# Kernel tuning notes

Hardware: AMD Instinct MI355X
Metric: run time of the kernel (lower is better)

## Reference

```python
import jax, jax.numpy as jnp
import numpy as np

B, S, V, E, H, L = 16, 256, 32000, 512, 1024, 2


def setup_inputs() -> dict:
    key = jax.random.key(0)
    ks = jax.random.split(key, 10)
    scale = 0.02
    tokens = jax.random.randint(ks[0], (B, S), 1, V)  # avoid pad token 0
    emb = jax.random.normal(ks[1], (V, E), dtype=jnp.float32) * scale
    W0 = jax.random.normal(ks[2], (E, 4 * H), dtype=jnp.float32) * scale
    U0 = jax.random.normal(ks[3], (H, 4 * H), dtype=jnp.float32) * scale
    b0 = jnp.zeros((4 * H,), dtype=jnp.float32)
    W1 = jax.random.normal(ks[4], (H, 4 * H), dtype=jnp.float32) * scale
    U1 = jax.random.normal(ks[5], (H, 4 * H), dtype=jnp.float32) * scale
    b1 = jnp.zeros((4 * H,), dtype=jnp.float32)
    Wd = jax.random.normal(ks[6], (H, V), dtype=jnp.float32) * scale
    bd = jnp.zeros((V,), dtype=jnp.float32)
    return {"tokens": tokens, "emb": emb, "W0": W0, "U0": U0, "b0": b0,
            "W1": W1, "U1": U1, "b1": b1, "Wd": Wd, "bd": bd}


def lstm_layer(x, mask, W, U, b):
    """Keras LSTM (gate order i,f,g,o), mask carries state/output on padded steps.
    x: [B,S,D], mask: [B,S] bool -> (ys [B,S,H], h [B,H], c [B,H])."""
    h_dim = U.shape[0]
    bsz = x.shape[0]
    x_t = jnp.swapaxes(x, 0, 1)           # [S,B,D]
    m_t = jnp.swapaxes(mask, 0, 1)        # [S,B]

    def step(carry, inp):
        h, c = carry
        xt, mt = inp
        z = xt @ W + h @ U + b            # [B,4H]
        i, f, g, o = jnp.split(z, 4, axis=-1)
        c_new = jax.nn.sigmoid(f) * c + jax.nn.sigmoid(i) * jnp.tanh(g)
        h_new = jax.nn.sigmoid(o) * jnp.tanh(c_new)
        mt = mt[:, None]
        h_new = jnp.where(mt, h_new, h)
        c_new = jnp.where(mt, c_new, c)
        return (h_new, c_new), h_new

    init = (jnp.zeros((bsz, h_dim), x.dtype), jnp.zeros((bsz, h_dim), x.dtype))
    (h, c), ys = jax.lax.scan(step, init, (x_t, m_t))
    return jnp.swapaxes(ys, 0, 1), h, c


def reference(tokens, emb, W0, U0, b0, W1, U1, b1, Wd, bd):
    mask = tokens != 0                    # mask_zero=True in Embedding
    x = emb[tokens]                       # [B,S,E]
    x, h0, c0 = lstm_layer(x, mask, W0, U0, b0)
    x, h1, c1 = lstm_layer(x, mask, W1, U1, b1)
    probs = jax.nn.softmax(x @ Wd + bd, axis=-1)  # Dense(softmax) -> [B,S,V]
    h_stack = jnp.stack([h0, h1])         # [L,B,H] final hidden states
    c_stack = jnp.stack([c0, c1])         # [L,B,H] final cell states
    return probs, h_stack, c_stack
```

## Files before the change

### kernel.cpp

```cpp
#include <hip/hip_runtime.h>

typedef __attribute__((ext_vector_type(8))) short bf16x8;
typedef __attribute__((ext_vector_type(4))) float f32x4;

#define S_LEN 256
#define VOCAB 32000
#define EMB   512
#define HID   1024

static const size_t OUT_H = 131072000ull;

__device__ inline unsigned short f2bf(float f) {
  unsigned int u = __float_as_uint(f);
  u = (u + 0x7FFFu + ((u >> 16) & 1u)) >> 16;
  return (unsigned short)u;
}
__device__ inline float bf2f(unsigned short s) {
  return __uint_as_float(((unsigned int)s) << 16);
}

__device__ inline void st_h(unsigned short* p, unsigned short v) {
  __hip_atomic_store(p, v, __ATOMIC_RELAXED, __HIP_MEMORY_SCOPE_AGENT);
}

__device__ inline int xcd_swz(int o, int n) {
  int q = n >> 3, r = n & 7;
  int x = o & 7, i = o >> 3;
  return (x < r ? x * (q + 1) : r * (q + 1) + (x - r) * q) + i;
}

__global__ __launch_bounds__(256) void k_transpose_bf16(const float* __restrict__ src,
                                                        unsigned short* __restrict__ dst,
                                                        int K, int N) {
  __shared__ float tile[64][65];
  int n0 = blockIdx.x * 64, k0 = blockIdx.y * 64;
  int tid = threadIdx.x;
#pragma unroll
  for (int i = 0; i < 16; ++i) {
    int e = tid + i * 256;
    int r = e >> 6, c = e & 63;
    tile[r][c] = src[(size_t)(k0 + r) * N + n0 + c];
  }
  __syncthreads();
#pragma unroll
  for (int i = 0; i < 16; ++i) {
    int e = tid + i * 256;
    int r = e >> 6, c = e & 63;
    dst[(size_t)(n0 + r) * K + k0 + c] = f2bf(tile[c][r]);
  }
}

__global__ __launch_bounds__(256) void k_gather_emb(const int* __restrict__ tokens,
                                                    const float* __restrict__ emb,
                                                    unsigned short* __restrict__ Xg) {
  int r = blockIdx.x;
  int s = r >> 4, b = r & 15;
  int tok = tokens[b * S_LEN + s];
  const float* src = emb + (size_t)tok * EMB;
  int k = threadIdx.x * 2;
  float2 v = *(const float2*)(src + k);
  ushort2 o; o.x = f2bf(v.x); o.y = f2bf(v.y);
  *(ushort2*)(Xg + (size_t)r * EMB + k) = o;
}

__device__ inline void gload16(const void* g, void* lds) {
  __builtin_amdgcn_global_load_lds((const __attribute__((address_space(1))) unsigned int*)g,
                                   (__attribute__((address_space(3))) unsigned int*)lds,
                                   16, 0, 0);
}

template <bool SMPART, bool BF16OUT>
__global__ __launch_bounds__(256) void k_gemm_bf16(const unsigned short* __restrict__ A,
                                                   const unsigned short* __restrict__ BT,
                                                   float* __restrict__ Cf,
                                                   unsigned short* __restrict__ Cb,
                                                   const float* __restrict__ bias,
                                                   int M, int N, int K,
                                                   float* __restrict__ Mpart,
                                                   float* __restrict__ Spart,
                                                   int NT) {
  __shared__ unsigned short As[4096];
  __shared__ unsigned short Bs[4096];
  __shared__ float redM[2][2][64];
  __shared__ float redS[2][2][64];
  int tid = threadIdx.x;
  int lane = tid & 63, wv = tid >> 6;
  int wr = wv >> 1, wc = wv & 1;
  int bxs = xcd_swz(blockIdx.x, gridDim.x);
  int am0 = blockIdx.y * 128, bn0 = bxs * 128;
  f32x4 zero = {0.f, 0.f, 0.f, 0.f};
  f32x4 acc[4][4];
#pragma unroll
  for (int m = 0; m < 4; ++m)
#pragma unroll
    for (int n = 0; n < 4; ++n) acc[m][n] = zero;
  int KT = K >> 5;
  int lr = lane & 15, kq = lane >> 4;
  for (int kt = 0; kt < KT; ++kt) {
    int k0 = kt << 5;
    __syncthreads();
#pragma unroll
    for (int c = 0; c < 2; ++c) {
      int t2 = c * 256 + tid;
      int row = t2 & 127, kg = t2 >> 7;
      gload16(A + (size_t)(am0 + row) * K + k0 + kg * 8, &As[(c * 256 + wv * 64) * 8]);
    }
#pragma unroll
    for (int c = 0; c < 2; ++c) {
      int t2 = c * 256 + tid;
      int row = t2 & 127, kg = t2 >> 7;
      gload16(BT + (size_t)(bn0 + row) * K + k0 + kg * 8, &Bs[(c * 256 + wv * 64) * 8]);
    }
    __syncthreads();
    const bf16x8* Ap = (const bf16x8*)As;
    const bf16x8* Bp = (const bf16x8*)Bs;
    bf16x8 af[4], bf[4];
#pragma unroll
    for (int m = 0; m < 4; ++m) af[m] = Ap[kq * 128 + wr * 64 + m * 16 + lr];
#pragma unroll
    for (int n = 0; n < 4; ++n) bf[n] = Bp[kq * 128 + wc * 64 + n * 16 + lr];
#pragma unroll
    for (int m = 0; m < 4; ++m)
#pragma unroll
      for (int n = 0; n < 4; ++n)
        acc[m][n] = __builtin_amdgcn_mfma_f32_16x16x32_bf16(af[m], bf[n], acc[m][n], 0, 0, 0);
  }
  float bvc[4];
#pragma unroll
  for (int n = 0; n < 4; ++n) {
    int col = bn0 + wc * 64 + n * 16 + lr;
    bvc[n] = bias ? bias[col] : 0.f;
  }
#pragma unroll
  for (int m = 0; m < 4; ++m)
#pragma unroll
    for (int n = 0; n < 4; ++n) {
      int col = bn0 + wc * 64 + n * 16 + lr;
#pragma unroll
      for (int q = 0; q < 4; ++q) {
        int row = am0 + wr * 64 + m * 16 + kq * 4 + q;
        if constexpr (BF16OUT)
          Cb[(size_t)row * N + col] = f2bf(acc[m][n][q] + bvc[n]);
        else
          Cf[(size_t)row * N + col] = acc[m][n][q] + bvc[n];
      }
    }
  if constexpr (SMPART) {
#pragma unroll
    for (int m = 0; m < 4; ++m)
#pragma unroll
      for (int q = 0; q < 4; ++q) {
        float mx = fmaxf(fmaxf(acc[m][0][q] + bvc[0], acc[m][1][q] + bvc[1]),
                         fmaxf(acc[m][2][q] + bvc[2], acc[m][3][q] + bvc[3]));
#pragma unroll
        for (int off = 1; off < 16; off <<= 1) mx = fmaxf(mx, __shfl_xor(mx, off));
        if (lr == 0) redM[wr][wc][m * 16 + kq * 4 + q] = mx;
      }
    __syncthreads();
#pragma unroll
    for (int m = 0; m < 4; ++m)
#pragma unroll
      for (int q = 0; q < 4; ++q) {
        int idx = m * 16 + kq * 4 + q;
        float mxF = fmaxf(redM[wr][0][idx], redM[wr][1][idx]);
        float s = __expf(acc[m][0][q] + bvc[0] - mxF) + __expf(acc[m][1][q] + bvc[1] - mxF) +
                  __expf(acc[m][2][q] + bvc[2] - mxF) + __expf(acc[m][3][q] + bvc[3] - mxF);
#pragma unroll
        for (int off = 1; off < 16; off <<= 1) s += __shfl_xor(s, off);
        if (lr == 0) redS[wr][wc][idx] = s;
      }
    __syncthreads();
    if (wc == 0 && lr == 0) {
#pragma unroll
      for (int m = 0; m < 4; ++m)
#pragma unroll
        for (int q = 0; q < 4; ++q) {
          int idx = m * 16 + kq * 4 + q;
          int row = am0 + wr * 64 + idx;
          Mpart[(size_t)row * NT + bxs] = fmaxf(redM[wr][0][idx], redM[wr][1][idx]);
          Spart[(size_t)row * NT + bxs] = redS[wr][0][idx] + redS[wr][1][idx];
        }
    }
  }
}

__global__ __launch_bounds__(256) void k_sm_combine(const float* __restrict__ Mp,
                                                    const float* __restrict__ Sp,
                                                    float* __restrict__ MS, int T) {
  int row = blockIdx.x * 4 + (threadIdx.x >> 6);
  int lane = threadIdx.x & 63;
  float mx = -3.4e38f;
  for (int i = lane; i < T; i += 64) mx = fmaxf(mx, Mp[(size_t)row * T + i]);
#pragma unroll
  for (int o = 32; o > 0; o >>= 1) mx = fmaxf(mx, __shfl_xor(mx, o));
  float s = 0.f;
  for (int i = lane; i < T; i += 64)
    s += Sp[(size_t)row * T + i] * __expf(Mp[(size_t)row * T + i] - mx);
#pragma unroll
  for (int o = 32; o > 0; o >>= 1) s += __shfl_xor(s, o);
  if (lane == 0) { MS[row * 2] = mx; MS[row * 2 + 1] = 1.f / s; }
}

__global__ __launch_bounds__(256) void k_sm_apply(float* __restrict__ data,
                                                  const float* __restrict__ MS) {
  const int total = 4096 * (VOCAB / 4);
  for (int idx = blockIdx.x * 256 + threadIdx.x; idx < total; idx += gridDim.x * 256) {
    int row = idx / (VOCAB / 4);
    float M = MS[row * 2], inv = MS[row * 2 + 1];
    float4 v = ((const float4*)data)[idx];
    v.x = __expf(v.x - M) * inv;
    v.y = __expf(v.y - M) * inv;
    v.z = __expf(v.z - M) * inv;
    v.w = __expf(v.w - M) * inv;
    ((float4*)data)[idx] = v;
  }
}

__global__ __launch_bounds__(256) void k_sm_apply_bf16(const unsigned short* __restrict__ lg,
                                                       float* __restrict__ probs,
                                                       const float* __restrict__ MS) {
  const int total = 4096 * (VOCAB / 4);
  for (int idx = blockIdx.x * 256 + threadIdx.x; idx < total; idx += gridDim.x * 256) {
    int row = idx / (VOCAB / 4);
    float M = MS[row * 2], inv = MS[row * 2 + 1];
    ushort4 v = ((const ushort4*)lg)[idx];
    float4 o;
    o.x = __expf(bf2f(v.x) - M) * inv;
    o.y = __expf(bf2f(v.y) - M) * inv;
    o.z = __expf(bf2f(v.z) - M) * inv;
    o.w = __expf(bf2f(v.w) - M) * inv;
    ((float4*)probs)[idx] = o;
  }
}

struct LstmSmem {
  unsigned short U0s[16384];
  unsigned short W1s[16384];
  unsigned short U1s[16384];
  float zA[4][16][16];
  float zB[4][16][16];
  float c0[16][4], h0f[16][4], c1[16][4], h1f[16][4];
  float b1s[16];
  short toks[16][256];
  unsigned short h0st[16][4], h1st[16][4];
};

__global__ __launch_bounds__(256, 1) void k_lstm(const int* __restrict__ tokens,
                                                 const float* __restrict__ XW,
                                                 const unsigned short* __restrict__ U0T,
                                                 const unsigned short* __restrict__ W1T,
                                                 const unsigned short* __restrict__ U1T,
                                                 const float* __restrict__ b1,
                                                 unsigned short* __restrict__ h0r,
                                                 unsigned short* __restrict__ h1r,
                                                 unsigned short* __restrict__ Y1,
                                                 float* outHC,
                                                 int* bar) {
  extern __shared__ char smraw[];
  LstmSmem& sm = *(LstmSmem*)smraw;
  int tid = threadIdx.x, bid = blockIdx.x;
  int lane = tid & 63, wv = tid >> 6;

  for (int idx = tid; idx < 2048; idx += 256) {
    int cidx = idx >> 7, kg = idx & 127;
    int gcol = (cidx >> 2) * 1024 + bid * 4 + (cidx & 3);
    *(uint4*)&sm.U0s[(kg * 16 + cidx) * 8] = *(const uint4*)&U0T[(size_t)gcol * 1024 + kg * 8];
    *(uint4*)&sm.W1s[(kg * 16 + cidx) * 8] = *(const uint4*)&W1T[(size_t)gcol * 1024 + kg * 8];
    *(uint4*)&sm.U1s[(kg * 16 + cidx) * 8] = *(const uint4*)&U1T[(size_t)gcol * 1024 + kg * 8];
  }
  for (int idx = tid; idx < 4096; idx += 256) {
    sm.toks[idx >> 8][idx & 255] = (short)tokens[idx];
  }
  if (tid < 64) {
    int b = tid >> 2, u = tid & 3;
    sm.c0[b][u] = 0.f; sm.h0f[b][u] = 0.f;
    sm.c1[b][u] = 0.f; sm.h1f[b][u] = 0.f;
  }
  if (tid < 16) sm.b1s[tid] = b1[(tid >> 2) * 1024 + bid * 4 + (tid & 3)];
  __syncthreads();

  int lr = lane & 15, kq = lane >> 4;

  auto gbar = [&](int gen) {
    __syncthreads();
    if (tid == 0)
      __hip_atomic_store(&bar[bid * 16], gen, __ATOMIC_RELAXED, __HIP_MEMORY_SCOPE_AGENT);
    int ok;
    do {
      int f = __hip_atomic_load(&bar[tid * 16], __ATOMIC_RELAXED, __HIP_MEMORY_SCOPE_AGENT);
      ok = (f >= gen);
    } while (!__syncthreads_and(ok));
  };

  if (wv == 1) {
    int l = tid - 64, b = l >> 2, u = l & 3;
    const float* xp = XW + (size_t)b * 4096 + bid * 4 + u;
    float z0 = xp[0], z2 = xp[2048], z3 = xp[3072];
    float ii = 1.f / (1.f + expf(-z0));
    float gg = tanhf(z2);
    float oo = 1.f / (1.f + expf(-z3));
    float cn = ii * gg;
    float hn = oo * tanhf(cn);
    if (sm.toks[b][0] == 0) { cn = 0.f; hn = 0.f; }
    sm.c0[b][u] = cn; sm.h0f[b][u] = hn;
    st_h(h0r + b * HID + bid * 4 + u, f2bf(hn));
  }
  gbar(1);

  for (int t = 0; t < 255; ++t) {
    const unsigned short* h0t = h0r + (size_t)t * 16384;
    const unsigned short* h1p = h1r + (size_t)(t > 0 ? t - 1 : 0) * 16384;
    unsigned short* h1c = h1r + (size_t)t * 16384;
    unsigned short* h0n = h0r + (size_t)(t + 1) * 16384;

    float xwv0 = 0, xwv1 = 0, xwv2 = 0, xwv3 = 0;
    if (wv == 1) {
      int l = tid - 64, b = l >> 2, u = l & 3;
      const float* xp = XW + ((size_t)(t + 1) * 16 + b) * 4096 + bid * 4 + u;
      xwv0 = xp[0]; xwv1 = xp[1024]; xwv2 = xp[2048]; xwv3 = xp[3072];
    }

    f32x4 accB = {0.f, 0.f, 0.f, 0.f};
    {
      const unsigned short* ap = (wv < 2) ? h0t : h1p;
      const unsigned short* bm = (wv < 2) ? sm.W1s : sm.U1s;
      int kofs = (wv & 1) * 512;
      if (wv < 2 || t > 0) {
#pragma unroll
        for (int s8 = 0; s8 < 16; ++s8) {
          int kb = kofs + s8 * 32;
          bf16x8 av = *(const bf16x8*)(ap + lr * HID + kb + kq * 8);
          bf16x8 bv = *(const bf16x8*)&bm[(((kb >> 3) + kq) * 16 + lr) * 8];
          accB = __builtin_amdgcn_mfma_f32_16x16x32_bf16(av, bv, accB, 0, 0, 0);
        }
      }
    }
    f32x4 accA = {0.f, 0.f, 0.f, 0.f};
#pragma unroll
    for (int s8 = 0; s8 < 8; ++s8) {
      int kb = wv * 256 + s8 * 32;
      bf16x8 av = *(const bf16x8*)(h0t + lr * HID + kb + kq * 8);
      bf16x8 bv = *(const bf16x8*)&sm.U0s[(((kb >> 3) + kq) * 16 + lr) * 8];
      accA = __builtin_amdgcn_mfma_f32_16x16x32_bf16(av, bv, accA, 0, 0, 0);
    }
#pragma unroll
    for (int q = 0; q < 4; ++q) {
      sm.zB[wv][kq * 4 + q][lr] = accB[q];
      sm.zA[wv][kq * 4 + q][lr] = accA[q];
    }
    __syncthreads();

    if (wv == 0) {
      int b = tid >> 2, u = tid & 3;
      int tok = sm.toks[b][t];
      float z0 = sm.b1s[0 + u]  + sm.zB[0][b][0 + u]  + sm.zB[1][b][0 + u]  + sm.zB[2][b][0 + u]  + sm.zB[3][b][0 + u];
      float z1 = sm.b1s[4 + u]  + sm.zB[0][b][4 + u]  + sm.zB[1][b][4 + u]  + sm.zB[2][b][4 + u]  + sm.zB[3][b][4 + u];
      float z2 = sm.b1s[8 + u]  + sm.zB[0][b][8 + u]  + sm.zB[1][b][8 + u]  + sm.zB[2][b][8 + u]  + sm.zB[3][b][8 + u];
      float z3 = sm.b1s[12 + u] + sm.zB[0][b][12 + u] + sm.zB[1][b][12 + u] + sm.zB[2][b][12 + u] + sm.zB[3][b][12 + u];
      float ii = 1.f / (1.f + expf(-z0));
      float ff = 1.f / (1.f + expf(-z1));
      float gg = tanhf(z2);
      float oo = 1.f / (1.f + expf(-z3));
      float cold = sm.c1[b][u], hold = sm.h1f[b][u];
      float cn = ff * cold + ii * gg;
      float hn = oo * tanhf(cn);
      if (tok == 0) { cn = cold; hn = hold; }
      sm.c1[b][u] = cn; sm.h1f[b][u] = hn;
      unsigned short hb = f2bf(hn);
      sm.h1st[b][u] = hb;
      Y1[((size_t)b * S_LEN + t) * HID + bid * 4 + u] = hb;
    } else if (wv == 1) {
      int l = tid - 64, b = l >> 2, u = l & 3;
      int tok = sm.toks[b][t + 1];
      float z0 = xwv0 + sm.zA[0][b][0 + u]  + sm.zA[1][b][0 + u]  + sm.zA[2][b][0 + u]  + sm.zA[3][b][0 + u];
      float z1 = xwv1 + sm.zA[0][b][4 + u]  + sm.zA[1][b][4 + u]  + sm.zA[2][b][4 + u]  + sm.zA[3][b][4 + u];
      float z2 = xwv2 + sm.zA[0][b][8 + u]  + sm.zA[1][b][8 + u]  + sm.zA[2][b][8 + u]  + sm.zA[3][b][8 + u];
      float z3 = xwv3 + sm.zA[0][b][12 + u] + sm.zA[1][b][12 + u] + sm.zA[2][b][12 + u] + sm.zA[3][b][12 + u];
      float ii = 1.f / (1.f + expf(-z0));
      float ff = 1.f / (1.f + expf(-z1));
      float gg = tanhf(z2);
      float oo = 1.f / (1.f + expf(-z3));
      float cold = sm.c0[b][u], hold = sm.h0f[b][u];
      float cn = ff * cold + ii * gg;
      float hn = oo * tanhf(cn);
      if (tok == 0) { cn = cold; hn = hold; }
      sm.c0[b][u] = cn; sm.h0f[b][u] = hn;
      sm.h0st[b][u] = f2bf(hn);
    }
    __syncthreads();
    if (tid < 32) {
      int b = tid & 15;
      unsigned long long v = *(const unsigned long long*)((tid < 16) ? &sm.h1st[b][0]
                                                                     : &sm.h0st[b][0]);
      unsigned short* dst = (tid < 16) ? (h1c + b * HID + bid * 4)
                                       : (h0n + b * HID + bid * 4);
      __hip_atomic_store((unsigned long long*)dst, v, __ATOMIC_RELAXED,
                         __HIP_MEMORY_SCOPE_AGENT);
    }
    gbar(t + 2);
  }

  {
    const unsigned short* h0t = h0r + 255ull * 16384;
    const unsigned short* h1p = h1r + 254ull * 16384;
    f32x4 accB = {0.f, 0.f, 0.f, 0.f};
    const unsigned short* ap = (wv < 2) ? h0t : h1p;
    const unsigned short* bm = (wv < 2) ? sm.W1s : sm.U1s;
    int kofs = (wv & 1) * 512;
#pragma unroll
    for (int s8 = 0; s8 < 16; ++s8) {
      int kb = kofs + s8 * 32;
      bf16x8 av = *(const bf16x8*)(ap + lr * HID + kb + kq * 8);
      bf16x8 bv = *(const bf16x8*)&bm[(((kb >> 3) + kq) * 16 + lr) * 8];
      accB = __builtin_amdgcn_mfma_f32_16x16x32_bf16(av, bv, accB, 0, 0, 0);
    }
#pragma unroll
    for (int q = 0; q < 4; ++q) sm.zB[wv][kq * 4 + q][lr] = accB[q];
    __syncthreads();
    if (wv == 0) {
      int b = tid >> 2, u = tid & 3;
      int tok = sm.toks[b][255];
      float z0 = sm.b1s[0 + u]  + sm.zB[0][b][0 + u]  + sm.zB[1][b][0 + u]  + sm.zB[2][b][0 + u]  + sm.zB[3][b][0 + u];
      float z1 = sm.b1s[4 + u]  + sm.zB[0][b][4 + u]  + sm.zB[1][b][4 + u]  + sm.zB[2][b][4 + u]  + sm.zB[3][b][4 + u];
      float z2 = sm.b1s[8 + u]  + sm.zB[0][b][8 + u]  + sm.zB[1][b][8 + u]  + sm.zB[2][b][8 + u]  + sm.zB[3][b][8 + u];
      float z3 = sm.b1s[12 + u] + sm.zB[0][b][12 + u] + sm.zB[1][b][12 + u] + sm.zB[2][b][12 + u] + sm.zB[3][b][12 + u];
      float ii = 1.f / (1.f + expf(-z0));
      float ff = 1.f / (1.f + expf(-z1));
      float gg = tanhf(z2);
      float oo = 1.f / (1.f + expf(-z3));
      float cold = sm.c1[b][u], hold = sm.h1f[b][u];
      float cn = ff * cold + ii * gg;
      float hn = oo * tanhf(cn);
      if (tok == 0) { cn = cold; hn = hold; }
      sm.c1[b][u] = cn; sm.h1f[b][u] = hn;
      Y1[((size_t)b * S_LEN + 255) * HID + bid * 4 + u] = f2bf(hn);
    }
    __syncthreads();
  }

  if (tid < 64) {
    int b = tid >> 2, u = tid & 3, ug = bid * 4 + u;
    outHC[OUT_H + (size_t)b * HID + ug]         = sm.h0f[b][u];
    outHC[OUT_H + 16384 + (size_t)b * HID + ug] = sm.h1f[b][u];
    outHC[OUT_H + 32768 + (size_t)b * HID + ug] = sm.c0[b][u];
    outHC[OUT_H + 49152 + (size_t)b * HID + ug] = sm.c1[b][u];
  }
}

extern "C" void kernel_launch(void* const* d_in, const int* in_sizes, int n_in,
                              void* d_out, int out_size, void* d_ws, size_t ws_size,
                              hipStream_t stream) {
  const int*   tokens = (const int*)d_in[0];
  const float* emb = (const float*)d_in[1];
  const float* W0  = (const float*)d_in[2];
  const float* U0  = (const float*)d_in[3];
  const float* b0  = (const float*)d_in[4];
  const float* W1  = (const float*)d_in[5];
  const float* U1  = (const float*)d_in[6];
  const float* b1  = (const float*)d_in[7];
  const float* Wd  = (const float*)d_in[8];
  const float* bd  = (const float*)d_in[9];
  float* out = (float*)d_out;

  char* ws = (char*)d_ws;
  size_t off = 0;
  auto alloc = [&](size_t bytes) { char* p = ws + off; off += (bytes + 255) & ~(size_t)255; return p; };
  unsigned short* W0T = (unsigned short*)alloc(4096ull * 512 * 2);
  unsigned short* U0T = (unsigned short*)alloc(4096ull * 1024 * 2);
  unsigned short* W1T = (unsigned short*)alloc(4096ull * 1024 * 2);
  unsigned short* U1T = (unsigned short*)alloc(4096ull * 1024 * 2);
  unsigned short* WdT = (unsigned short*)alloc(32000ull * 1024 * 2);
  unsigned short* Xg  = (unsigned short*)alloc(4096ull * 512 * 2);
  unsigned short* Y1  = (unsigned short*)alloc(4096ull * 1024 * 2);
  int*   bar   = (int*)alloc(16384);
  float* Mpart = (float*)alloc(4096ull * 250 * 4);
  float* Spart = (float*)alloc(4096ull * 250 * 4);
  float* MS    = (float*)alloc(4096ull * 2 * 4);
  unsigned short* Lb = nullptr;
  if (ws_size >= off + 4096ull * VOCAB * 2 + 256)
    Lb = (unsigned short*)alloc(4096ull * VOCAB * 2);

  float* XW = out;
  unsigned short* h0r = (unsigned short*)((char*)d_out + 192ull * 1024 * 1024);
  unsigned short* h1r = (unsigned short*)((char*)d_out + 208ull * 1024 * 1024);

  hipMemsetAsync(bar, 0, 16384, stream);

  hipFuncSetAttribute((const void*)k_lstm, hipFuncAttributeMaxDynamicSharedMemorySize,
                      (int)sizeof(LstmSmem));

  k_transpose_bf16<<<dim3(64, 8), 256, 0, stream>>>(W0, W0T, 512, 4096);
  k_transpose_bf16<<<dim3(64, 16), 256, 0, stream>>>(U0, U0T, 1024, 4096);
  k_transpose_bf16<<<dim3(64, 16), 256, 0, stream>>>(W1, W1T, 1024, 4096);
  k_transpose_bf16<<<dim3(64, 16), 256, 0, stream>>>(U1, U1T, 1024, 4096);
  k_transpose_bf16<<<dim3(500, 16), 256, 0, stream>>>(Wd, WdT, 1024, 32000);
  k_gather_emb<<<4096, 256, 0, stream>>>(tokens, emb, Xg);

  k_gemm_bf16<false, false><<<dim3(32, 32), 256, 0, stream>>>(Xg, W0T, XW, nullptr, b0,
                                                              4096, 4096, 512,
                                                              nullptr, nullptr, 0);

  k_lstm<<<256, 256, sizeof(LstmSmem), stream>>>(tokens, XW, U0T, W1T, U1T, b1,
                                                 h0r, h1r, Y1, out, bar);

  if (Lb) {
    k_gemm_bf16<true, true><<<dim3(250, 32), 256, 0, stream>>>(Y1, WdT, nullptr, Lb, bd,
                                                               4096, 32000, 1024,
                                                               Mpart, Spart, 250);
    k_sm_combine<<<1024, 256, 0, stream>>>(Mpart, Spart, MS, 250);
    k_sm_apply_bf16<<<4096, 256, 0, stream>>>(Lb, out, MS);
  } else {
    k_gemm_bf16<true, false><<<dim3(250, 32), 256, 0, stream>>>(Y1, WdT, out, nullptr, bd,
                                                                4096, 32000, 1024,
                                                                Mpart, Spart, 250);
    k_sm_combine<<<1024, 256, 0, stream>>>(Mpart, Spart, MS, 250);
    k_sm_apply<<<4096, 256, 0, stream>>>(out, MS);
  }
}
```

Before: 2.363 ms.

## Replace vocab-projection GEMM with 256x256-tile pipelined kernel using swizzled LDS

Splits the GEMM into a plain 128-tile kernel for the input projection and a new 256x256-tile, 512-thread kernel for the output projection. The new kernel uses 64-wide K steps, double-buffered direct-to-LDS loads with an XOR swizzle to avoid bank conflicts, and interleaves loads with MFMA work using barriers and wave priority. The larger tile halves the number of softmax partials and raises arithmetic intensity. It also always uses the bf16 logits buffer, removing the fp32 fallback path. That path assumes the workspace is large enough, and the 128KB of LDS per block may limit occupancy.

Measured after the change: 2.150 ms. 1.1x faster.

```diff
diff --git a/kernel.cpp b/kernel.cpp
--- a/kernel.cpp
+++ b/kernel.cpp
@@ -27,6 +27,12 @@
   int q = n >> 3, r = n & 7;
   int x = o & 7, i = o >> 3;
   return (x < r ? x * (q + 1) : r * (q + 1) + (x - r) * q) + i;
+}
+
+__device__ inline void gload16(const void* g, void* lds) {
+  __builtin_amdgcn_global_load_lds((const __attribute__((address_space(1))) unsigned int*)g,
+                                   (__attribute__((address_space(3))) unsigned int*)lds,
+                                   16, 0, 0);
 }
 
 __global__ __launch_bounds__(256) void k_transpose_bf16(const float* __restrict__ src,
@@ -63,26 +69,13 @@
   *(ushort2*)(Xg + (size_t)r * EMB + k) = o;
 }
 
-__device__ inline void gload16(const void* g, void* lds) {
-  __builtin_amdgcn_global_load_lds((const __attribute__((address_space(1))) unsigned int*)g,
-                                   (__attribute__((address_space(3))) unsigned int*)lds,
-                                   16, 0, 0);
-}
-
-template <bool SMPART, bool BF16OUT>
-__global__ __launch_bounds__(256) void k_gemm_bf16(const unsigned short* __restrict__ A,
-                                                   const unsigned short* __restrict__ BT,
-                                                   float* __restrict__ Cf,
-                                                   unsigned short* __restrict__ Cb,
-                                                   const float* __restrict__ bias,
-                                                   int M, int N, int K,
-                                                   float* __restrict__ Mpart,
-                                                   float* __restrict__ Spart,
-                                                   int NT) {
+__global__ __launch_bounds__(256) void k_gemm128(const unsigned short* __restrict__ A,
+                                                 const unsigned short* __restrict__ BT,
+                                                 float* __restrict__ C,
+                                                 const float* __restrict__ bias,
+                                                 int M, int N, int K) {
   __shared__ unsigned short As[4096];
   __shared__ unsigned short Bs[4096];
-  __shared__ float redM[2][2][64];
-  __shared__ float redS[2][2][64];
   int tid = threadIdx.x;
   int lane = tid & 63, wv = tid >> 6;
   int wr = wv >> 1, wc = wv & 1;
@@ -125,62 +118,192 @@
       for (int n = 0; n < 4; ++n)
         acc[m][n] = __builtin_amdgcn_mfma_f32_16x16x32_bf16(af[m], bf[n], acc[m][n], 0, 0, 0);
   }
-  float bvc[4];
-#pragma unroll
-  for (int n = 0; n < 4; ++n) {
-    int col = bn0 + wc * 64 + n * 16 + lr;
-    bvc[n] = bias ? bias[col] : 0.f;
-  }
 #pragma unroll
   for (int m = 0; m < 4; ++m)
 #pragma unroll
     for (int n = 0; n < 4; ++n) {
       int col = bn0 + wc * 64 + n * 16 + lr;
+      float bv = bias ? bias[col] : 0.f;
 #pragma unroll
       for (int q = 0; q < 4; ++q) {
         int row = am0 + wr * 64 + m * 16 + kq * 4 + q;
-        if constexpr (BF16OUT)
-          Cb[(size_t)row * N + col] = f2bf(acc[m][n][q] + bvc[n]);
-        else
-          Cf[(size_t)row * N + col] = acc[m][n][q] + bvc[n];
+        C[(size_t)row * N + col] = acc[m][n][q] + bv;
       }
     }
-  if constexpr (SMPART) {
-#pragma unroll
-    for (int m = 0; m < 4; ++m)
+}
+
+__global__ __launch_bounds__(512, 2) void k_gemm256(const unsigned short* __restrict__ A,
+                                                    const unsigned short* __restrict__ BT,
+                                                    unsigned short* __restrict__ Cb,
+                                                    const float* __restrict__ bias,
+                                                    int M, int N, int K,
+                                                    float* __restrict__ Mpart,
+                                                    float* __restrict__ Spart,
+                                                    int NT) {
+  extern __shared__ unsigned short lds[];
+  int tid = threadIdx.x;
+  int w = tid >> 6, lane = tid & 63;
+  int wr = w >> 2, wcn = w & 3;
+  int lr = lane & 15, kq = lane >> 4, sw = lr & 7;
+  int bxs = xcd_swz(blockIdx.x, gridDim.x);
+  int gm0 = blockIdx.y * 256, gn0 = bxs * 256;
+  const int KT = K >> 6;
+
+  f32x4 acc[8][4];
+#pragma unroll
+  for (int m = 0; m < 8; ++m)
+#pragma unroll
+    for (int n = 0; n < 4; ++n) acc[m][n] = f32x4{0.f, 0.f, 0.f, 0.f};
+
+  auto stage = [&](const unsigned short* g, int grow0, int kt, int mat, int half) {
+    unsigned short* sb = lds + ((((kt & 1) * 2 + mat) * 2 + half) << 13);
+#pragma unroll
+    for (int ld = 0; ld < 2; ++ld) {
+      int j = ld * 512 + tid;
+      int row = j >> 3, c16 = j & 7;
+      const unsigned short* src =
+          g + (size_t)(grow0 + half * 128 + row) * K + kt * 64 + ((c16 ^ (row & 7)) << 3);
+      gload16(src, sb + ((ld * 512 + w * 64) << 3));
+    }
+  };
+
+  stage(A, gm0, 0, 0, 0); stage(A, gm0, 0, 0, 1);
+  stage(BT, gn0, 0, 1, 0); stage(BT, gn0, 0, 1, 1);
+  stage(BT, gn0, 1, 1, 0); stage(BT, gn0, 1, 1, 1);
+  asm volatile("s_waitcnt vmcnt(4)" ::: "memory");
+  __builtin_amdgcn_sched_barrier(0);
+  __builtin_amdgcn_s_barrier();
+
+  const int halfB = wcn >> 1;
+  const int rowB0 = (wcn & 1) * 64;
+
+  for (int i = 0; i < KT / 2; ++i) {
+    int kt0 = 2 * i, kt1 = 2 * i + 1;
+#pragma unroll
+    for (int half = 0; half < 2; ++half) {
+      int kt = half ? kt1 : kt0;
+      int buf = kt & 1;
+      const unsigned short* ldsA = lds + (((buf * 2 + 0) * 2 + wr) << 13);
+      const unsigned short* ldsB = lds + (((buf * 2 + 1) * 2 + halfB) << 13);
+      bf16x8 bf[4][2];
+#pragma unroll
+      for (int qd = 0; qd < 4; ++qd) {
+        if (qd == 0) {
+#pragma unroll
+          for (int fn = 0; fn < 4; ++fn)
+#pragma unroll
+            for (int kk = 0; kk < 2; ++kk) {
+              int r = rowB0 + fn * 16 + lr;
+              int c = (kk * 4 + kq) ^ sw;
+              bf[fn][kk] = *(const bf16x8*)(ldsB + r * 64 + c * 8);
+            }
+        }
+        bf16x8 af[2][2];
+#pragma unroll
+        for (int m2 = 0; m2 < 2; ++m2)
+#pragma unroll
+          for (int kk = 0; kk < 2; ++kk) {
+            int r = (qd * 2 + m2) * 16 + lr;
+            int c = (kk * 4 + kq) ^ sw;
+            af[m2][kk] = *(const bf16x8*)(ldsA + r * 64 + c * 8);
+          }
+        if (half == 0) {
+          if (qd == 0) { stage(A, gm0, kt0 + 1, 0, 0); stage(A, gm0, kt0 + 1, 0, 1); }
+          else if (qd == 1) { if (kt0 + 2 < KT) stage(BT, gn0, kt0 + 2, 1, 0); }
+          else if (qd == 2) { if (kt0 + 2 < KT) stage(BT, gn0, kt0 + 2, 1, 1); }
+          else {
+            if (kt0 + 2 < KT) asm volatile("s_waitcnt vmcnt(4)" ::: "memory");
+            else              asm volatile("s_waitcnt vmcnt(0)" ::: "memory");
+          }
+        } else {
+          if (qd == 0)      { if (kt1 + 1 < KT) stage(A, gm0, kt1 + 1, 0, 0); }
+          else if (qd == 1) { if (kt1 + 1 < KT) stage(A, gm0, kt1 + 1, 0, 1); }
+          else if (qd == 2) { if (kt1 + 2 < KT) stage(BT, gn0, kt1 + 2, 1, 0); }
+          else {
+            if (kt1 + 2 < KT) { stage(BT, gn0, kt1 + 2, 1, 1);
+                                asm volatile("s_waitcnt vmcnt(4)" ::: "memory"); }
+            else              asm volatile("s_waitcnt vmcnt(0)" ::: "memory");
+          }
+        }
+        __builtin_amdgcn_sched_barrier(0);
+        __builtin_amdgcn_s_barrier();
+        asm volatile("s_waitcnt lgkmcnt(0)" ::: "memory");
+        __builtin_amdgcn_sched_barrier(0);
+        __builtin_amdgcn_s_setprio(1);
+#pragma unroll
+        for (int m2 = 0; m2 < 2; ++m2)
+#pragma unroll
+          for (int n = 0; n < 4; ++n)
+#pragma unroll
+            for (int kk = 0; kk < 2; ++kk)
+              acc[qd * 2 + m2][n] =
+                  __builtin_amdgcn_mfma_f32_16x16x32_bf16(af[m2][kk], bf[n][kk],
+                                                          acc[qd * 2 + m2][n], 0, 0, 0);
+        __builtin_amdgcn_s_setprio(0);
+        __builtin_amdgcn_sched_barrier(0);
+        __builtin_amdgcn_s_barrier();
+      }
+    }
+  }
+
+  asm volatile("s_waitcnt vmcnt(0) lgkmcnt(0)" ::: "memory");
+  __syncthreads();
+
+  float bvc[4];
+#pragma unroll
+  for (int n = 0; n < 4; ++n) bvc[n] = bias[gn0 + wcn * 64 + n * 16 + lr];
+#pragma unroll
+  for (int fm = 0; fm < 8; ++fm)
+#pragma unroll
+    for (int n = 0; n < 4; ++n) {
+      int col = gn0 + wcn * 64 + n * 16 + lr;
 #pragma unroll
       for (int q = 0; q < 4; ++q) {
-        float mx = fmaxf(fmaxf(acc[m][0][q] + bvc[0], acc[m][1][q] + bvc[1]),
-                         fmaxf(acc[m][2][q] + bvc[2], acc[m][3][q] + bvc[3]));
-#pragma unroll
-        for (int off = 1; off < 16; off <<= 1) mx = fmaxf(mx, __shfl_xor(mx, off));
-        if (lr == 0) redM[wr][wc][m * 16 + kq * 4 + q] = mx;
+        int row = gm0 + wr * 128 + fm * 16 + kq * 4 + q;
+        Cb[(size_t)row * N + col] = f2bf(acc[fm][n][q] + bvc[n]);
       }
-    __syncthreads();
-#pragma unroll
-    for (int m = 0; m < 4; ++m)
+    }
+  float* redM = (float*)lds;
+  float* redS = (float*)lds + 1024;
+#pragma unroll
+  for (int fm = 0; fm < 8; ++fm)
+#pragma unroll
+    for (int q = 0; q < 4; ++q) {
+      float mx = fmaxf(fmaxf(acc[fm][0][q] + bvc[0], acc[fm][1][q] + bvc[1]),
+                       fmaxf(acc[fm][2][q] + bvc[2], acc[fm][3][q] + bvc[3]));
+#pragma unroll
+      for (int off = 1; off < 16; off <<= 1) mx = fmaxf(mx, __shfl_xor(mx, off));
+      if (lr == 0) redM[(wr * 4 + wcn) * 128 + fm * 16 + kq * 4 + q] = mx;
+    }
+  __syncthreads();
+#pragma unroll
+  for (int fm = 0; fm < 8; ++fm)
+#pragma unroll
+    for (int q = 0; q < 4; ++q) {
+      int idx = fm * 16 + kq * 4 + q;
+      float mxF = fmaxf(fmaxf(redM[(wr * 4 + 0) * 128 + idx], redM[(wr * 4 + 1) * 128 + idx]),
+                        fmaxf(redM[(wr * 4 + 2) * 128 + idx], redM[(wr * 4 + 3) * 128 + idx]));
+      float s = __expf(acc[fm][0][q] + bvc[0] - mxF) + __expf(acc[fm][1][q] + bvc[1] - mxF) +
+                __expf(acc[fm][2][q] + bvc[2] - mxF) + __expf(acc[fm][3][q] + bvc[3] - mxF);
+#pragma unroll
+      for (int off = 1; off < 16; off <<= 1) s += __shfl_xor(s, off);
+      if (lr == 0) redS[(wr * 4 + wcn) * 128 + idx] = s;
+    }
+  __syncthreads();
+  if (wcn == 0 && lr == 0) {
+#pragma unroll
+    for (int fm = 0; fm < 8; ++fm)
 #pragma unroll
       for (int q = 0; q < 4; ++q) {
-        int idx = m * 16 + kq * 4 + q;
-        float mxF = fmaxf(redM[wr][0][idx], redM[wr][1][idx]);
-        float s = __expf(acc[m][0][q] + bvc[0] - mxF) + __expf(acc[m][1][q] + bvc[1] - mxF) +
-                  __expf(acc[m][2][q] + bvc[2] - mxF) + __expf(acc[m][3][q] + bvc[3] - mxF);
-#pragma unroll
-        for (int off = 1; off < 16; off <<= 1) s += __shfl_xor(s, off);
-        if (lr == 0) redS[wr][wc][idx] = s;
+        int idx = fm * 16 + kq * 4 + q;
+        float mxF = fmaxf(fmaxf(redM[(wr * 4 + 0) * 128 + idx], redM[(wr * 4 + 1) * 128 + idx]),
+                          fmaxf(redM[(wr * 4 + 2) * 128 + idx], redM[(wr * 4 + 3) * 128 + idx]));
+        float ss = redS[(wr * 4 + 0) * 128 + idx] + redS[(wr * 4 + 1) * 128 + idx] +
+                   redS[(wr * 4 + 2) * 128 + idx] + redS[(wr * 4 + 3) * 128 + idx];
+        int row = gm0 + wr * 128 + idx;
+        Mpart[(size_t)row * NT + bxs] = mxF;
+        Spart[(size_t)row * NT + bxs] = ss;
       }
-    __syncthreads();
-    if (wc == 0 && lr == 0) {
-#pragma unroll
-      for (int m = 0; m < 4; ++m)
-#pragma unroll
-        for (int q = 0; q < 4; ++q) {
-          int idx = m * 16 + kq * 4 + q;
-          int row = am0 + wr * 64 + idx;
-          Mpart[(size_t)row * NT + bxs] = fmaxf(redM[wr][0][idx], redM[wr][1][idx]);
-          Spart[(size_t)row * NT + bxs] = redS[wr][0][idx] + redS[wr][1][idx];
-        }
-    }
   }
 }
 
@@ -199,21 +322,6 @@
 #pragma unroll
   for (int o = 32; o > 0; o >>= 1) s += __shfl_xor(s, o);
   if (lane == 0) { MS[row * 2] = mx; MS[row * 2 + 1] = 1.f / s; }
-}
-
-__global__ __launch_bounds__(256) void k_sm_apply(float* __restrict__ data,
-                                                  const float* __restrict__ MS) {
-  const int total = 4096 * (VOCAB / 4);
-  for (int idx = blockIdx.x * 256 + threadIdx.x; idx < total; idx += gridDim.x * 256) {
-    int row = idx / (VOCAB / 4);
-    float M = MS[row * 2], inv = MS[row * 2 + 1];
-    float4 v = ((const float4*)data)[idx];
-    v.x = __expf(v.x - M) * inv;
-    v.y = __expf(v.y - M) * inv;
-    v.z = __expf(v.z - M) * inv;
-    v.w = __expf(v.w - M) * inv;
-    ((float4*)data)[idx] = v;
-  }
 }
 
 __global__ __launch_bounds__(256) void k_sm_apply_bf16(const unsigned short* __restrict__ lg,
@@ -473,12 +581,10 @@
   unsigned short* Xg  = (unsigned short*)alloc(4096ull * 512 * 2);
   unsigned short* Y1  = (unsigned short*)alloc(4096ull * 1024 * 2);
   int*   bar   = (int*)alloc(16384);
-  float* Mpart = (float*)alloc(4096ull * 250 * 4);
-  float* Spart = (float*)alloc(4096ull * 250 * 4);
+  float* Mpart = (float*)alloc(4096ull * 125 * 4);
+  float* Spart = (float*)alloc(4096ull * 125 * 4);
   float* MS    = (float*)alloc(4096ull * 2 * 4);
-  unsigned short* Lb = nullptr;
-  if (ws_size >= off + 4096ull * VOCAB * 2 + 256)
-    Lb = (unsigned short*)alloc(4096ull * VOCAB * 2);
+  unsigned short* Lb = (unsigned short*)alloc(4096ull * VOCAB * 2);
 
   float* XW = out;
   unsigned short* h0r = (unsigned short*)((char*)d_out + 192ull * 1024 * 1024);
@@ -488,6 +594,8 @@
 
   hipFuncSetAttribute((const void*)k_lstm, hipFuncAttributeMaxDynamicSharedMemorySize,
                       (int)sizeof(LstmSmem));
+  hipFuncSetAttribute((const void*)k_gemm256, hipFuncAttributeMaxDynamicSharedMemorySize,
+                      131072);
 
   k_transpose_bf16<<<dim3(64, 8), 256, 0, stream>>>(W0, W0T, 512, 4096);
   k_transpose_bf16<<<dim3(64, 16), 256, 0, stream>>>(U0, U0T, 1024, 4096);
@@ -496,24 +604,13 @@
   k_transpose_bf16<<<dim3(500, 16), 256, 0, stream>>>(Wd, WdT, 1024, 32000);
   k_gather_emb<<<4096, 256, 0, stream>>>(tokens, emb, Xg);
 
-  k_gemm_bf16<false, false><<<dim3(32, 32), 256, 0, stream>>>(Xg, W0T, XW, nullptr, b0,
-                                                              4096, 4096, 512,
-                                                              nullptr, nullptr, 0);
+  k_gemm128<<<dim3(32, 32), 256, 0, stream>>>(Xg, W0T, XW, b0, 4096, 4096, 512);
 
   k_lstm<<<256, 256, sizeof(LstmSmem), stream>>>(tokens, XW, U0T, W1T, U1T, b1,
                                                  h0r, h1r, Y1, out, bar);
 
-  if (Lb) {
-    k_gemm_bf16<true, true><<<dim3(250, 32), 256, 0, stream>>>(Y1, WdT, nullptr, Lb, bd,
-                                                               4096, 32000, 1024,
-                                                               Mpart, Spart, 250);
-    k_sm_combine<<<1024, 256, 0, stream>>>(Mpart, Spart, MS, 250);
-    k_sm_apply_bf16<<<4096, 256, 0, stream>>>(Lb, out, MS);
-  } else {
-    k_gemm_bf16<true, false><<<dim3(250, 32), 256, 0, stream>>>(Y1, WdT, out, nullptr, bd,
-                                                                4096, 32000, 1024,
-                                                                Mpart, Spart, 250);
-    k_sm_combine<<<1024, 256, 0, stream>>>(Mpart, Spart, MS, 250);
-    k_sm_apply<<<4096, 256, 0, stream>>>(out, MS);
-  }
-}
+  k_gemm256<<<dim3(125, 16), 512, 131072, stream>>>(Y1, WdT, Lb, bd, 4096, 32000, 1024,
+                                                    Mpart, Spart, 125);
+  k_sm_combine<<<1024, 256, 0, stream>>>(Mpart, Spart, MS, 125);
+  k_sm_apply_bf16<<<4096, 256, 0, stream>>>(Lb, out, MS);
+}
```
